# Performance work log

Hardware: AMD Instinct MI355X
Metric: run time of the kernel (lower is better)

The kernel has to match this reference:

```python
import jax, jax.numpy as jnp
import numpy as np

N, E = 20000, 160000
D_IN, HID, HEADS = 256, 64, 10
NEG_SLOPE = 0.2


def setup_inputs() -> dict:
    key = jax.random.key(0)
    ks = jax.random.split(key, 12)
    s = 0.05
    f = jnp.float32
    return {
        "x": jax.random.normal(ks[0], (N, D_IN), f),
        "edge_index": jax.random.randint(ks[1], (2, E), 0, N, jnp.int32),
        # GATConv 1: in=D_IN, out=HID, heads=10, concat=True
        "W1": (jax.random.normal(ks[2], (D_IN, HEADS * HID), f) * s),
        "a_src1": (jax.random.normal(ks[3], (HEADS, HID), f) * s),
        "a_dst1": (jax.random.normal(ks[4], (HEADS, HID), f) * s),
        "b1": jnp.zeros((HEADS * HID,), f),
        # GATConv 2: in=HEADS*HID, out=HID, heads=1
        "W2": (jax.random.normal(ks[5], (HEADS * HID, HID), f) * s),
        "a_src2": (jax.random.normal(ks[6], (1, HID), f) * s),
        "a_dst2": (jax.random.normal(ks[7], (1, HID), f) * s),
        "b2": jnp.zeros((HID,), f),
        # final Linear(hidden_dim, hidden_dim)
        "Wfc": (jax.random.normal(ks[8], (HID, HID), f) * s),
        "bfc": jnp.zeros((HID,), f),
    }


def gat_conv(x, src, dst, n, W, a_src, a_dst, b, heads, concat):
    """PyG GATConv (eval mode): gather, leaky-relu scores, segment softmax, scatter."""
    c = W.shape[1] // heads
    h = (x @ W).reshape(n, heads, c)                      # [N, H, C]
    score_src = jnp.sum(h * a_src, axis=-1)               # [N, H]
    score_dst = jnp.sum(h * a_dst, axis=-1)               # [N, H]
    e = jax.nn.leaky_relu(score_src[src] + score_dst[dst], NEG_SLOPE)  # [E, H]
    # segment softmax over incoming edges of each dst node
    m = jax.ops.segment_max(e, dst, num_segments=n)
    e = jnp.exp(e - m[dst])
    denom = jax.ops.segment_sum(e, dst, num_segments=n)
    alpha = e / (denom[dst] + 1e-16)                      # [E, H]
    msg = alpha[:, :, None] * h[src]                      # [E, H, C]
    out = jax.ops.segment_sum(msg, dst, num_segments=n)   # [N, H, C]
    out = out.reshape(n, heads * c) if concat else out.mean(axis=1)
    return out + b


def reference(x, edge_index, W1, a_src1, a_dst1, b1, W2, a_src2, a_dst2, b2, Wfc, bfc):
    n = x.shape[0]
    # add self loops (PyG default)
    loops = jnp.arange(n, dtype=edge_index.dtype)
    src = jnp.concatenate([edge_index[0], loops])
    dst = jnp.concatenate([edge_index[1], loops])
    h = jax.nn.relu(gat_conv(x, src, dst, n, W1, a_src1, a_dst1, b1, HEADS, True))
    h = jax.nn.relu(gat_conv(h, src, dst, n, W2, a_src2, a_dst2, b2, 1, True))
    return jax.nn.relu(h @ Wfc + bfc)
```

## Files before the change

### kernel.cpp

```cpp
#include <hip/hip_runtime.h>
#include <cstdint>
#include <cstddef>

constexpr int N_NODES = 20000;
constexpr int E_EDGES = 160000;
constexpr int D_INC   = 256;
constexpr int HEADSC  = 10;
constexpr int EN      = E_EDGES + N_NODES;
constexpr int ELLW    = 96;
constexpr float NEG_SLOPE = 0.2f;

typedef _Float16 half8 __attribute__((ext_vector_type(8)));
typedef _Float16 half4v __attribute__((ext_vector_type(4)));
typedef float f32x4 __attribute__((ext_vector_type(4)));

__global__ __launch_bounds__(256) void gemm1_k(
    const _Float16* __restrict__ A,
    const _Float16* __restrict__ BT,
    _Float16* __restrict__ C,
    const float* __restrict__ asv, const float* __restrict__ adv,
    float* __restrict__ s_s, float* __restrict__ s_d, int M)
{
    __shared__ alignas(16) _Float16 Ah[64][72];
    __shared__ alignas(16) _Float16 Bh[128][72];
    const int tid = threadIdx.x;
    const int wv  = tid >> 6;
    const int ln  = tid & 63;
    const int row0 = blockIdx.y * 64;
    const int col0 = blockIdx.x * 128;
    const int m = ln & 15;
    const int q = ln >> 4;
    const int arow = tid >> 2;
    const int acg  = (tid & 3) * 16;
    const int brow = tid >> 1;
    const int bcg  = (tid & 1) * 32;

    const int ar_c = min(row0 + arow, M - 1);
    const _Float16* aptr = A  + (size_t)ar_c * 256 + acg;
    const _Float16* bptr = BT + (size_t)(col0 + brow) * 256 + bcg;

    int4 a0, a1, bv0, bv1, bv2, bv3;
    a0  = *reinterpret_cast<const int4*>(aptr);
    a1  = *reinterpret_cast<const int4*>(aptr + 8);
    bv0 = *reinterpret_cast<const int4*>(bptr);
    bv1 = *reinterpret_cast<const int4*>(bptr + 8);
    bv2 = *reinterpret_cast<const int4*>(bptr + 16);
    bv3 = *reinterpret_cast<const int4*>(bptr + 24);

    f32x4 acc[8] = {};

    for (int k0 = 0; k0 < 256; k0 += 64) {
        *reinterpret_cast<int4*>(&Ah[arow][acg])      = a0;
        *reinterpret_cast<int4*>(&Ah[arow][acg + 8])  = a1;
        *reinterpret_cast<int4*>(&Bh[brow][bcg])      = bv0;
        *reinterpret_cast<int4*>(&Bh[brow][bcg + 8])  = bv1;
        *reinterpret_cast<int4*>(&Bh[brow][bcg + 16]) = bv2;
        *reinterpret_cast<int4*>(&Bh[brow][bcg + 24]) = bv3;
        __syncthreads();

        if (k0 + 64 < 256) {
            const _Float16* ap = aptr + k0 + 64;
            a0 = *reinterpret_cast<const int4*>(ap);
            a1 = *reinterpret_cast<const int4*>(ap + 8);
            const _Float16* bp = bptr + k0 + 64;
            bv0 = *reinterpret_cast<const int4*>(bp);
            bv1 = *reinterpret_cast<const int4*>(bp + 8);
            bv2 = *reinterpret_cast<const int4*>(bp + 16);
            bv3 = *reinterpret_cast<const int4*>(bp + 24);
        }

#pragma unroll
        for (int ks = 0; ks < 2; ++ks) {
            const half8 af = *reinterpret_cast<const half8*>(
                &Ah[wv * 16 + m][ks * 32 + q * 8]);
#pragma unroll
            for (int ct = 0; ct < 8; ++ct) {
                const half8 bf = *reinterpret_cast<const half8*>(
                    &Bh[ct * 16 + m][ks * 32 + q * 8]);
                acc[ct] = __builtin_amdgcn_mfma_f32_16x16x32_f16(af, bf, acc[ct],
                                                                 0, 0, 0);
            }
        }
        __syncthreads();
    }

#pragma unroll
    for (int ct = 0; ct < 8; ++ct) {
        const int col  = col0 + ct * 16 + m;
        const int head = col >> 6;
        const int cw   = col & 63;
        _Float16* cp = C + (size_t)head * N_NODES * 64 + cw;
#pragma unroll
        for (int r = 0; r < 4; ++r) {
            const int row = row0 + wv * 16 + q * 4 + r;
            if (row < M)
                cp[(size_t)row * 64] = (_Float16)acc[ct][r];
        }
    }

    const int h0i = blockIdx.x * 2;
    float pa[2][4] = {}, pd[2][4] = {};
#pragma unroll
    for (int ct = 0; ct < 8; ++ct) {
        const int hh = ct >> 2;
        const int ch = (ct & 3) * 16 + m;
        const float a_ = asv[(h0i + hh) * 64 + ch];
        const float d_ = adv[(h0i + hh) * 64 + ch];
#pragma unroll
        for (int r = 0; r < 4; ++r) {
            pa[hh][r] += acc[ct][r] * a_;
            pd[hh][r] += acc[ct][r] * d_;
        }
    }
#pragma unroll
    for (int o = 1; o < 16; o <<= 1) {
#pragma unroll
        for (int hh = 0; hh < 2; ++hh)
#pragma unroll
            for (int r = 0; r < 4; ++r) {
                pa[hh][r] += __shfl_xor(pa[hh][r], o, 64);
                pd[hh][r] += __shfl_xor(pd[hh][r], o, 64);
            }
    }
    if (m == 0) {
#pragma unroll
        for (int hh = 0; hh < 2; ++hh)
#pragma unroll
            for (int r = 0; r < 4; ++r) {
                const int row = row0 + wv * 16 + q * 4 + r;
                if (row < M) {
                    s_s[(size_t)(h0i + hh) * N_NODES + row] = pa[hh][r];
                    s_d[(size_t)(h0i + hh) * N_NODES + row] = pd[hh][r];
                }
            }
    }
}

__global__ __launch_bounds__(128) void gemm2_k(
    const _Float16* __restrict__ A,
    const _Float16* __restrict__ BT,
    _Float16* __restrict__ C,
    const float* __restrict__ asv, const float* __restrict__ adv,
    float* __restrict__ s_s, float* __restrict__ s_d)
{
    __shared__ alignas(16) _Float16 Ah[32][72];
    __shared__ alignas(16) _Float16 Bh[64][72];
    const int tid = threadIdx.x;
    const int wv  = tid >> 6;
    const int ln  = tid & 63;
    const int row0 = blockIdx.x * 32;
    const int m = ln & 15;
    const int q = ln >> 4;
    const int arow = tid >> 2;
    const int acg  = (tid & 3) * 16;
    const int brow = tid >> 1;
    const int bcg  = (tid & 1) * 32;

    const _Float16* aptr = A  + (size_t)(row0 + arow) * 640 + acg;
    const _Float16* bptr = BT + (size_t)brow * 640 + bcg;

    int4 a0, a1, b0, b1, b2, b3;
    a0 = *reinterpret_cast<const int4*>(aptr);
    a1 = *reinterpret_cast<const int4*>(aptr + 8);
    b0 = *reinterpret_cast<const int4*>(bptr);
    b1 = *reinterpret_cast<const int4*>(bptr + 8);
    b2 = *reinterpret_cast<const int4*>(bptr + 16);
    b3 = *reinterpret_cast<const int4*>(bptr + 24);

    f32x4 acc[4] = {};

    for (int k0 = 0; k0 < 640; k0 += 64) {
        *reinterpret_cast<int4*>(&Ah[arow][acg])      = a0;
        *reinterpret_cast<int4*>(&Ah[arow][acg + 8])  = a1;
        *reinterpret_cast<int4*>(&Bh[brow][bcg])      = b0;
        *reinterpret_cast<int4*>(&Bh[brow][bcg + 8])  = b1;
        *reinterpret_cast<int4*>(&Bh[brow][bcg + 16]) = b2;
        *reinterpret_cast<int4*>(&Bh[brow][bcg + 24]) = b3;
        __syncthreads();

        if (k0 + 64 < 640) {
            const _Float16* ap = aptr + k0 + 64;
            a0 = *reinterpret_cast<const int4*>(ap);
            a1 = *reinterpret_cast<const int4*>(ap + 8);
            const _Float16* bp = bptr + k0 + 64;
            b0 = *reinterpret_cast<const int4*>(bp);
            b1 = *reinterpret_cast<const int4*>(bp + 8);
            b2 = *reinterpret_cast<const int4*>(bp + 16);
            b3 = *reinterpret_cast<const int4*>(bp + 24);
        }

#pragma unroll
        for (int ks = 0; ks < 2; ++ks) {
            const half8 af = *reinterpret_cast<const half8*>(
                &Ah[wv * 16 + m][ks * 32 + q * 8]);
#pragma unroll
            for (int ct = 0; ct < 4; ++ct) {
                const half8 bf = *reinterpret_cast<const half8*>(
                    &Bh[ct * 16 + m][ks * 32 + q * 8]);
                acc[ct] = __builtin_amdgcn_mfma_f32_16x16x32_f16(af, bf, acc[ct],
                                                                 0, 0, 0);
            }
        }
        __syncthreads();
    }

#pragma unroll
    for (int ct = 0; ct < 4; ++ct) {
#pragma unroll
        for (int r = 0; r < 4; ++r) {
            const int row = row0 + wv * 16 + q * 4 + r;
            C[(size_t)row * 64 + ct * 16 + m] = (_Float16)acc[ct][r];
        }
    }

    float pa[4] = {}, pd[4] = {};
#pragma unroll
    for (int ct = 0; ct < 4; ++ct) {
        const float a_ = asv[ct * 16 + m];
        const float d_ = adv[ct * 16 + m];
#pragma unroll
        for (int r = 0; r < 4; ++r) {
            pa[r] += acc[ct][r] * a_;
            pd[r] += acc[ct][r] * d_;
        }
    }
#pragma unroll
    for (int o = 1; o < 16; o <<= 1) {
#pragma unroll
        for (int r = 0; r < 4; ++r) {
            pa[r] += __shfl_xor(pa[r], o, 64);
            pd[r] += __shfl_xor(pd[r], o, 64);
        }
    }
    if (m == 0) {
#pragma unroll
        for (int r = 0; r < 4; ++r) {
            const int row = row0 + wv * 16 + q * 4 + r;
            s_s[row] = pa[r];
            s_d[row] = pd[r];
        }
    }
}

constexpr int XQ   = N_NODES * D_INC / 4;
constexpr int W1E  = D_INC * 640;
constexpr int W2E  = 640 * 64;
constexpr int WFCE = 64 * 64;
constexpr int SETUP_TOT = EN + XQ + W1E + W2E + WFCE;

__global__ void setup_k(const int* __restrict__ src, const int* __restrict__ dst,
                        int* __restrict__ deg, short* __restrict__ ell,
                        const float* __restrict__ x, const float* __restrict__ W1,
                        const float* __restrict__ W2, const float* __restrict__ Wfc,
                        _Float16* __restrict__ x16, _Float16* __restrict__ W1T,
                        _Float16* __restrict__ W2T, _Float16* __restrict__ WfcT)
{
    const int i = blockIdx.x * 256 + threadIdx.x;
    if (i < EN) {
        const int base = deg[N_NODES];
        int d, s;
        if (i < E_EDGES) { d = dst[i]; s = src[i]; }
        else             { d = i - E_EDGES; s = d; }
        const int r = atomicAdd(&deg[d], 1) - base;
        if ((unsigned)r < (unsigned)ELLW) ell[(size_t)d * ELLW + r] = (short)s;
    } else if (i < EN + XQ) {
        const int j = i - EN;
        const float4 v = reinterpret_cast<const float4*>(x)[j];
        half4v o = {(_Float16)v.x, (_Float16)v.y, (_Float16)v.z, (_Float16)v.w};
        reinterpret_cast<half4v*>(x16)[j] = o;
    } else if (i < EN + XQ + W1E) {
        const int j = i - EN - XQ;
        const int k = j / 640, n = j - k * 640;
        W1T[(size_t)n * D_INC + k] = (_Float16)W1[j];
    } else if (i < EN + XQ + W1E + W2E) {
        const int j = i - EN - XQ - W1E;
        const int k = j / 64, n = j - k * 64;
        W2T[(size_t)n * 640 + k] = (_Float16)W2[j];
    } else if (i < SETUP_TOT) {
        const int j = i - EN - XQ - W1E - W2E;
        const int k = j >> 6, n = j & 63;
        WfcT[(size_t)n * 64 + k] = (_Float16)Wfc[j];
    }
}

__global__ __launch_bounds__(256) void agg1_shard_k(
    const _Float16* __restrict__ h,
    const float* __restrict__ s_s,
    const float* __restrict__ s_d,
    const int* __restrict__ deg,
    const short* __restrict__ ell,
    const float* __restrict__ bias,
    _Float16* __restrict__ outp)
{
    const int b = blockIdx.x;
    int s, g;
    if (b < 5000) { s = b & 7; g = b >> 3; }
    else { const int c = b - 5000; s = 8 + (c & 1); g = c >> 1; }
    const int tid = threadIdx.x;
    const int nl  = tid >> 3;
    const int lc  = tid & 7;
    const int n   = g * 32 + nl;
    const _Float16* __restrict__ hb = h + (size_t)s * N_NODES * 64 + lc * 8;
    const float* __restrict__ ssh = s_s + (size_t)s * N_NODES;
    const short* __restrict__ row = ell + (size_t)n * ELLW;
    const float sd = s_d[(size_t)s * N_NODES + n];
    const int dbase = deg[N_NODES];
    const int dc = min(deg[n] - dbase, ELLW);

    float acc[8] = {};
    float den = 0.f;
    int i = 0;
    for (; i + 3 < dc; i += 4) {
        int sv[4];
#pragma unroll
        for (int u = 0; u < 4; ++u)
            sv[u] = (int)__builtin_nontemporal_load(row + i + u);
        float gv[4];
#pragma unroll
        for (int u = 0; u < 4; ++u) gv[u] = ssh[sv[u]];
        half8 vv[4];
#pragma unroll
        for (int u = 0; u < 4; ++u)
            vv[u] = *reinterpret_cast<const half8*>(hb + (size_t)sv[u] * 64);
        float w[4];
#pragma unroll
        for (int u = 0; u < 4; ++u) {
            float e = gv[u] + sd;
            e = (e > 0.f) ? e : NEG_SLOPE * e;
            w[u] = __expf(e);
            den += w[u];
        }
#pragma unroll
        for (int u = 0; u < 4; ++u)
#pragma unroll
            for (int j = 0; j < 8; ++j) acc[j] += w[u] * (float)vv[u][j];
    }
    for (; i < dc; ++i) {
        const int s0 = (int)__builtin_nontemporal_load(row + i);
        const float g0 = ssh[s0];
        const half8 v0 = *reinterpret_cast<const half8*>(hb + (size_t)s0 * 64);
        float e0 = g0 + sd;
        e0 = (e0 > 0.f) ? e0 : NEG_SLOPE * e0;
        const float w0 = __expf(e0);
        den += w0;
#pragma unroll
        for (int j = 0; j < 8; ++j) acc[j] += w0 * (float)v0[j];
    }
    const float inv = 1.f / (den + 1e-16f);
    const float* bb = bias + s * 64 + lc * 8;
    half8 o;
#pragma unroll
    for (int j = 0; j < 8; ++j)
        o[j] = (_Float16)fmaxf(acc[j] * inv + bb[j], 0.f);
    __builtin_nontemporal_store(
        o, reinterpret_cast<half8*>(outp + (size_t)n * 640 + s * 64 + lc * 8));
}

__global__ __launch_bounds__(256) void agg2fc_k(
    const _Float16* __restrict__ h,
    const float* __restrict__ s_s, const float* __restrict__ s_d,
    const int* __restrict__ deg, const short* __restrict__ ell,
    const float* __restrict__ b2,
    const _Float16* __restrict__ WfcT,
    const float* __restrict__ bfc,
    float* __restrict__ out)
{
    __shared__ alignas(16) _Float16 Os[32][72];
    const int tid = threadIdx.x;
    const int n0  = blockIdx.x * 32;
    const int nl  = tid >> 3;
    const int oct = tid & 7;
    const int n   = n0 + nl;

    {
        const _Float16* __restrict__ hb = h + oct * 8;
        const short* __restrict__ row = ell + (size_t)n * ELLW;
        const float sd = s_d[n];
        const int dbase = deg[N_NODES];
        const int dc = min(deg[n] - dbase, ELLW);

        float acc[8] = {};
        float den = 0.f;
        int i = 0;
        for (; i + 3 < dc; i += 4) {
            int   sv[4];
            float gv[4];
            half8 hv[4];
#pragma unroll
            for (int u = 0; u < 4; ++u) sv[u] = (int)row[i + u];
#pragma unroll
            for (int u = 0; u < 4; ++u) gv[u] = s_s[sv[u]];
#pragma unroll
            for (int u = 0; u < 4; ++u)
                hv[u] = *reinterpret_cast<const half8*>(hb + (size_t)sv[u] * 64);
#pragma unroll
            for (int u = 0; u < 4; ++u) {
                float e = gv[u] + sd;
                e = (e > 0.f) ? e : NEG_SLOPE * e;
                const float w = __expf(e);
                den += w;
#pragma unroll
                for (int j = 0; j < 8; ++j) acc[j] += w * (float)hv[u][j];
            }
        }
        for (; i < dc; ++i) {
            const int s0 = (int)row[i];
            const float g0 = s_s[s0];
            const half8 v0 = *reinterpret_cast<const half8*>(hb + (size_t)s0 * 64);
            float e0 = g0 + sd;
            e0 = (e0 > 0.f) ? e0 : NEG_SLOPE * e0;
            const float w0 = __expf(e0);
            den += w0;
#pragma unroll
            for (int j = 0; j < 8; ++j) acc[j] += w0 * (float)v0[j];
        }
        const float inv = 1.f / (den + 1e-16f);
        const float* bb = b2 + oct * 8;
        half8 o;
#pragma unroll
        for (int j = 0; j < 8; ++j)
            o[j] = (_Float16)fmaxf(acc[j] * inv + bb[j], 0.f);
        *reinterpret_cast<half8*>(&Os[nl][oct * 8]) = o;
    }
    __syncthreads();

    const int wv = tid >> 6;
    const int ln = tid & 63;
    if (wv < 2) {
        const int m = ln & 15;
        const int q = ln >> 4;
        f32x4 acc[4] = {};
#pragma unroll
        for (int ks = 0; ks < 2; ++ks) {
            const half8 af = *reinterpret_cast<const half8*>(
                &Os[wv * 16 + m][ks * 32 + q * 8]);
#pragma unroll
            for (int ct = 0; ct < 4; ++ct) {
                const half8 bf = *reinterpret_cast<const half8*>(
                    WfcT + (size_t)(ct * 16 + m) * 64 + ks * 32 + q * 8);
                acc[ct] = __builtin_amdgcn_mfma_f32_16x16x32_f16(af, bf, acc[ct],
                                                                 0, 0, 0);
            }
        }
#pragma unroll
        for (int ct = 0; ct < 4; ++ct) {
#pragma unroll
            for (int r = 0; r < 4; ++r) {
                const int row = n0 + wv * 16 + q * 4 + r;
                const int col = ct * 16 + m;
                out[(size_t)row * 64 + col] = fmaxf(acc[ct][r] + bfc[col], 0.f);
            }
        }
    }
}

extern "C" void kernel_launch(void* const* d_in, const int* in_sizes, int n_in,
                              void* d_out, int out_size, void* d_ws, size_t ws_size,
                              hipStream_t stream)
{
    const float* x      = (const float*)d_in[0];
    const int*   edges  = (const int*)d_in[1];
    const float* W1     = (const float*)d_in[2];
    const float* a_src1 = (const float*)d_in[3];
    const float* a_dst1 = (const float*)d_in[4];
    const float* b1     = (const float*)d_in[5];
    const float* W2     = (const float*)d_in[6];
    const float* a_src2 = (const float*)d_in[7];
    const float* a_dst2 = (const float*)d_in[8];
    const float* b2     = (const float*)d_in[9];
    const float* Wfc    = (const float*)d_in[10];
    const float* bfc    = (const float*)d_in[11];
    float* out = (float*)d_out;

    const int* src = edges;
    const int* dst = edges + E_EDGES;

    char* ws = (char*)d_ws;
    size_t off = 0;
    auto alloc = [&](size_t bytes) -> void* {
        void* p = ws + off;
        off += (bytes + 255) & ~(size_t)255;
        return p;
    };
    _Float16*  h1   = (_Float16*)alloc((size_t)N_NODES * 640 * sizeof(_Float16));
    _Float16*  out1 = (_Float16*)alloc((size_t)N_NODES * 640 * sizeof(_Float16));
    _Float16*  h2   = (_Float16*)alloc((size_t)N_NODES * 64 * sizeof(_Float16));
    _Float16*  x16  = (_Float16*)alloc((size_t)N_NODES * D_INC * sizeof(_Float16));
    _Float16*  W1T  = (_Float16*)alloc((size_t)640 * D_INC * sizeof(_Float16));
    _Float16*  W2T  = (_Float16*)alloc((size_t)64 * 640 * sizeof(_Float16));
    _Float16*  WfcT = (_Float16*)alloc((size_t)64 * 64 * sizeof(_Float16));
    float*     ss1  = (float*)alloc((size_t)N_NODES * HEADSC * sizeof(float));
    float*     sd1  = (float*)alloc((size_t)N_NODES * HEADSC * sizeof(float));
    float*     ss2  = (float*)alloc((size_t)N_NODES * sizeof(float));
    float*     sd2  = (float*)alloc((size_t)N_NODES * sizeof(float));
    int*       deg  = (int*)alloc((size_t)(N_NODES + 1) * sizeof(int));
    short*     ell  = (short*)alloc((size_t)N_NODES * ELLW * sizeof(short));

    setup_k<<<(SETUP_TOT + 255) / 256, 256, 0, stream>>>(
        src, dst, deg, ell, x, W1, W2, Wfc, x16, W1T, W2T, WfcT);

    dim3 g1(5, (N_NODES + 63) / 64);
    gemm1_k<<<g1, 256, 0, stream>>>(x16, W1T, h1, a_src1, a_dst1,
                                    ss1, sd1, N_NODES);

    agg1_shard_k<<<6250, 256, 0, stream>>>(h1, ss1, sd1, deg, ell, b1, out1);

    gemm2_k<<<N_NODES / 32, 128, 0, stream>>>(out1, W2T, h2, a_src2, a_dst2,
                                              ss2, sd2);

    agg2fc_k<<<N_NODES / 32, 256, 0, stream>>>(h2, ss2, sd2, deg, ell,
                                               b2, WfcT, bfc, out);
}
```

Measured before the change: 188.8 us.

## Recompute source attention scores from gathered features instead of precomputed table

The GEMM kernels no longer compute or store per-node source scores. The aggregation kernels instead recompute each edge's source score as a dot product of the already-gathered fp16 feature row with a_src, reduced across 8 lanes with shuffles. Edge indices are also loaded as one 4-wide vector. This removes a dependent random gather into the score array and its write traffic, at the cost of extra FMAs and shuffles per edge and scores computed from fp16-rounded features.

After: 206.0 us. +9.1%, slower.

```diff
diff --git a/kernel.cpp b/kernel.cpp
--- a/kernel.cpp
+++ b/kernel.cpp
@@ -13,13 +13,14 @@
 typedef _Float16 half8 __attribute__((ext_vector_type(8)));
 typedef _Float16 half4v __attribute__((ext_vector_type(4)));
 typedef float f32x4 __attribute__((ext_vector_type(4)));
+typedef short short4v __attribute__((ext_vector_type(4)));
 
 __global__ __launch_bounds__(256) void gemm1_k(
     const _Float16* __restrict__ A,
     const _Float16* __restrict__ BT,
     _Float16* __restrict__ C,
-    const float* __restrict__ asv, const float* __restrict__ adv,
-    float* __restrict__ s_s, float* __restrict__ s_d, int M)
+    const float* __restrict__ adv,
+    float* __restrict__ s_d, int M)
 {
     __shared__ alignas(16) _Float16 Ah[64][72];
     __shared__ alignas(16) _Float16 Bh[128][72];
@@ -99,28 +100,23 @@
     }
 
     const int h0i = blockIdx.x * 2;
-    float pa[2][4] = {}, pd[2][4] = {};
+    float pd[2][4] = {};
 #pragma unroll
     for (int ct = 0; ct < 8; ++ct) {
         const int hh = ct >> 2;
         const int ch = (ct & 3) * 16 + m;
-        const float a_ = asv[(h0i + hh) * 64 + ch];
         const float d_ = adv[(h0i + hh) * 64 + ch];
 #pragma unroll
-        for (int r = 0; r < 4; ++r) {
-            pa[hh][r] += acc[ct][r] * a_;
+        for (int r = 0; r < 4; ++r)
             pd[hh][r] += acc[ct][r] * d_;
-        }
     }
 #pragma unroll
     for (int o = 1; o < 16; o <<= 1) {
 #pragma unroll
         for (int hh = 0; hh < 2; ++hh)
 #pragma unroll
-            for (int r = 0; r < 4; ++r) {
-                pa[hh][r] += __shfl_xor(pa[hh][r], o, 64);
+            for (int r = 0; r < 4; ++r)
                 pd[hh][r] += __shfl_xor(pd[hh][r], o, 64);
-            }
     }
     if (m == 0) {
 #pragma unroll
@@ -128,10 +124,8 @@
 #pragma unroll
             for (int r = 0; r < 4; ++r) {
                 const int row = row0 + wv * 16 + q * 4 + r;
-                if (row < M) {
-                    s_s[(size_t)(h0i + hh) * N_NODES + row] = pa[hh][r];
+                if (row < M)
                     s_d[(size_t)(h0i + hh) * N_NODES + row] = pd[hh][r];
-                }
             }
     }
 }
@@ -140,8 +134,8 @@
     const _Float16* __restrict__ A,
     const _Float16* __restrict__ BT,
     _Float16* __restrict__ C,
-    const float* __restrict__ asv, const float* __restrict__ adv,
-    float* __restrict__ s_s, float* __restrict__ s_d)
+    const float* __restrict__ adv,
+    float* __restrict__ s_d)
 {
     __shared__ alignas(16) _Float16 Ah[32][72];
     __shared__ alignas(16) _Float16 Bh[64][72];
@@ -213,30 +207,24 @@
         }
     }
 
-    float pa[4] = {}, pd[4] = {};
+    float pd[4] = {};
 #pragma unroll
     for (int ct = 0; ct < 4; ++ct) {
-        const float a_ = asv[ct * 16 + m];
         const float d_ = adv[ct * 16 + m];
 #pragma unroll
-        for (int r = 0; r < 4; ++r) {
-            pa[r] += acc[ct][r] * a_;
+        for (int r = 0; r < 4; ++r)
             pd[r] += acc[ct][r] * d_;
-        }
     }
 #pragma unroll
     for (int o = 1; o < 16; o <<= 1) {
 #pragma unroll
-        for (int r = 0; r < 4; ++r) {
-            pa[r] += __shfl_xor(pa[r], o, 64);
+        for (int r = 0; r < 4; ++r)
             pd[r] += __shfl_xor(pd[r], o, 64);
-        }
     }
     if (m == 0) {
 #pragma unroll
         for (int r = 0; r < 4; ++r) {
             const int row = row0 + wv * 16 + q * 4 + r;
-            s_s[row] = pa[r];
             s_d[row] = pd[r];
         }
     }
@@ -285,7 +273,7 @@
 
 __global__ __launch_bounds__(256) void agg1_shard_k(
     const _Float16* __restrict__ h,
-    const float* __restrict__ s_s,
+    const float* __restrict__ asv,
     const float* __restrict__ s_d,
     const int* __restrict__ deg,
     const short* __restrict__ ell,
@@ -301,9 +289,11 @@
     const int lc  = tid & 7;
     const int n   = g * 32 + nl;
     const _Float16* __restrict__ hb = h + (size_t)s * N_NODES * 64 + lc * 8;
-    const float* __restrict__ ssh = s_s + (size_t)s * N_NODES;
     const short* __restrict__ row = ell + (size_t)n * ELLW;
     const float sd = s_d[(size_t)s * N_NODES + n];
+    float av[8];
+#pragma unroll
+    for (int j = 0; j < 8; ++j) av[j] = asv[s * 64 + lc * 8 + j];
     const int dbase = deg[N_NODES];
     const int dc = min(deg[n] - dbase, ELLW);
 
@@ -311,40 +301,43 @@
     float den = 0.f;
     int i = 0;
     for (; i + 3 < dc; i += 4) {
-        int sv[4];
+        const short4v qi = __builtin_nontemporal_load(
+            reinterpret_cast<const short4v*>(row + i));
+        half8 vv[4];
 #pragma unroll
         for (int u = 0; u < 4; ++u)
-            sv[u] = (int)__builtin_nontemporal_load(row + i + u);
-        float gv[4];
-#pragma unroll
-        for (int u = 0; u < 4; ++u) gv[u] = ssh[sv[u]];
-        half8 vv[4];
-#pragma unroll
-        for (int u = 0; u < 4; ++u)
-            vv[u] = *reinterpret_cast<const half8*>(hb + (size_t)sv[u] * 64);
-        float w[4];
+            vv[u] = *reinterpret_cast<const half8*>(hb + (size_t)(int)qi[u] * 64);
 #pragma unroll
         for (int u = 0; u < 4; ++u) {
-            float e = gv[u] + sd;
+            float p = 0.f;
+#pragma unroll
+            for (int j = 0; j < 8; ++j) p += av[j] * (float)vv[u][j];
+            p += __shfl_xor(p, 1, 64);
+            p += __shfl_xor(p, 2, 64);
+            p += __shfl_xor(p, 4, 64);
+            float e = p + sd;
             e = (e > 0.f) ? e : NEG_SLOPE * e;
-            w[u] = __expf(e);
-            den += w[u];
-        }
-#pragma unroll
-        for (int u = 0; u < 4; ++u)
-#pragma unroll
-            for (int j = 0; j < 8; ++j) acc[j] += w[u] * (float)vv[u][j];
+            const float w = __expf(e);
+            den += w;
+#pragma unroll
+            for (int j = 0; j < 8; ++j) acc[j] += w * (float)vv[u][j];
+        }
     }
     for (; i < dc; ++i) {
         const int s0 = (int)__builtin_nontemporal_load(row + i);
-        const float g0 = ssh[s0];
         const half8 v0 = *reinterpret_cast<const half8*>(hb + (size_t)s0 * 64);
-        float e0 = g0 + sd;
-        e0 = (e0 > 0.f) ? e0 : NEG_SLOPE * e0;
-        const float w0 = __expf(e0);
-        den += w0;
-#pragma unroll
-        for (int j = 0; j < 8; ++j) acc[j] += w0 * (float)v0[j];
+        float p = 0.f;
+#pragma unroll
+        for (int j = 0; j < 8; ++j) p += av[j] * (float)v0[j];
+        p += __shfl_xor(p, 1, 64);
+        p += __shfl_xor(p, 2, 64);
+        p += __shfl_xor(p, 4, 64);
+        float e = p + sd;
+        e = (e > 0.f) ? e : NEG_SLOPE * e;
+        const float w = __expf(e);
+        den += w;
+#pragma unroll
+        for (int j = 0; j < 8; ++j) acc[j] += w * (float)v0[j];
     }
     const float inv = 1.f / (den + 1e-16f);
     const float* bb = bias + s * 64 + lc * 8;
@@ -358,7 +351,8 @@
 
 __global__ __launch_bounds__(256) void agg2fc_k(
     const _Float16* __restrict__ h,
-    const float* __restrict__ s_s, const float* __restrict__ s_d,
+    const float* __restrict__ asv,
+    const float* __restrict__ s_d,
     const int* __restrict__ deg, const short* __restrict__ ell,
     const float* __restrict__ b2,
     const _Float16* __restrict__ WfcT,
@@ -376,6 +370,9 @@
         const _Float16* __restrict__ hb = h + oct * 8;
         const short* __restrict__ row = ell + (size_t)n * ELLW;
         const float sd = s_d[n];
+        float av[8];
+#pragma unroll
+        for (int j = 0; j < 8; ++j) av[j] = asv[oct * 8 + j];
         const int dbase = deg[N_NODES];
         const int dc = min(deg[n] - dbase, ELLW);
 
@@ -383,19 +380,22 @@
         float den = 0.f;
         int i = 0;
         for (; i + 3 < dc; i += 4) {
-            int   sv[4];
-            float gv[4];
+            const short4v qi = __builtin_nontemporal_load(
+                reinterpret_cast<const short4v*>(row + i));
             half8 hv[4];
 #pragma unroll
-            for (int u = 0; u < 4; ++u) sv[u] = (int)row[i + u];
-#pragma unroll
-            for (int u = 0; u < 4; ++u) gv[u] = s_s[sv[u]];
-#pragma unroll
             for (int u = 0; u < 4; ++u)
-                hv[u] = *reinterpret_cast<const half8*>(hb + (size_t)sv[u] * 64);
+                hv[u] = *reinterpret_cast<const half8*>(
+                    hb + (size_t)(int)qi[u] * 64);
 #pragma unroll
             for (int u = 0; u < 4; ++u) {
-                float e = gv[u] + sd;
+                float p = 0.f;
+#pragma unroll
+                for (int j = 0; j < 8; ++j) p += av[j] * (float)hv[u][j];
+                p += __shfl_xor(p, 1, 64);
+                p += __shfl_xor(p, 2, 64);
+                p += __shfl_xor(p, 4, 64);
+                float e = p + sd;
                 e = (e > 0.f) ? e : NEG_SLOPE * e;
                 const float w = __expf(e);
                 den += w;
@@ -405,14 +405,19 @@
         }
         for (; i < dc; ++i) {
             const int s0 = (int)row[i];
-            const float g0 = s_s[s0];
             const half8 v0 = *reinterpret_cast<const half8*>(hb + (size_t)s0 * 64);
-            float e0 = g0 + sd;
-            e0 = (e0 > 0.f) ? e0 : NEG_SLOPE * e0;
-            const float w0 = __expf(e0);
-            den += w0;
-#pragma unroll
-            for (int j = 0; j < 8; ++j) acc[j] += w0 * (float)v0[j];
+            float p = 0.f;
+#pragma unroll
+            for (int j = 0; j < 8; ++j) p += av[j] * (float)v0[j];
+            p += __shfl_xor(p, 1, 64);
+            p += __shfl_xor(p, 2, 64);
+            p += __shfl_xor(p, 4, 64);
+            float e = p + sd;
+            e = (e > 0.f) ? e : NEG_SLOPE * e;
+            const float w = __expf(e);
+            den += w;
+#pragma unroll
+            for (int j = 0; j < 8; ++j) acc[j] += w * (float)v0[j];
         }
         const float inv = 1.f / (den + 1e-16f);
         const float* bb = b2 + oct * 8;
@@ -489,9 +494,7 @@
     _Float16*  W1T  = (_Float16*)alloc((size_t)640 * D_INC * sizeof(_Float16));
     _Float16*  W2T  = (_Float16*)alloc((size_t)64 * 640 * sizeof(_Float16));
     _Float16*  WfcT = (_Float16*)alloc((size_t)64 * 64 * sizeof(_Float16));
-    float*     ss1  = (float*)alloc((size_t)N_NODES * HEADSC * sizeof(float));
     float*     sd1  = (float*)alloc((size_t)N_NODES * HEADSC * sizeof(float));
-    float*     ss2  = (float*)alloc((size_t)N_NODES * sizeof(float));
     float*     sd2  = (float*)alloc((size_t)N_NODES * sizeof(float));
     int*       deg  = (int*)alloc((size_t)(N_NODES + 1) * sizeof(int));
     short*     ell  = (short*)alloc((size_t)N_NODES * ELLW * sizeof(short));
@@ -500,14 +503,12 @@
         src, dst, deg, ell, x, W1, W2, Wfc, x16, W1T, W2T, WfcT);
 
     dim3 g1(5, (N_NODES + 63) / 64);
-    gemm1_k<<<g1, 256, 0, stream>>>(x16, W1T, h1, a_src1, a_dst1,
-                                    ss1, sd1, N_NODES);
-
-    agg1_shard_k<<<6250, 256, 0, stream>>>(h1, ss1, sd1, deg, ell, b1, out1);
-
-    gemm2_k<<<N_NODES / 32, 128, 0, stream>>>(out1, W2T, h2, a_src2, a_dst2,
-                                              ss2, sd2);
-
-    agg2fc_k<<<N_NODES / 32, 256, 0, stream>>>(h2, ss2, sd2, deg, ell,
+    gemm1_k<<<g1, 256, 0, stream>>>(x16, W1T, h1, a_dst1, sd1, N_NODES);
+
+    agg1_shard_k<<<6250, 256, 0, stream>>>(h1, a_src1, sd1, deg, ell, b1, out1);
+
+    gemm2_k<<<N_NODES / 32, 128, 0, stream>>>(out1, W2T, h2, a_dst2, sd2);
+
+    agg2fc_k<<<N_NODES / 32, 256, 0, stream>>>(h2, a_src2, sd2, deg, ell,
                                                b2, WfcT, bfc, out);
 }
```
